# Optimization experiments

Measured on AMD Instinct MI355X. Metric: run time of the kernel, lower is better.

Reference implementation:

```python
import jax, jax.numpy as jnp
import numpy as np

BIG = 1e10  # sentinel depth for empty pixels


def setup_inputs() -> dict:
    key = jax.random.key(0)
    k1, k2, k3, k4, k5 = jax.random.split(key, 5)
    N, C = 200000, 64
    B, H, W = 4, 376, 1241
    features = jax.random.normal(k1, (N, C), dtype=jnp.float32)
    # coordinates: [batch_id, z, y, x]; grid is ~67 bins per axis given
    # voxel_size=0.75 and pcd_range [0,-25,-25,50,25,25]
    b = jax.random.randint(k2, (N, 1), 0, B, dtype=jnp.int32)
    z = jax.random.randint(k3, (N, 1), 0, 67, dtype=jnp.int32)
    y = jax.random.randint(k4, (N, 1), 0, 67, dtype=jnp.int32)
    x = jax.random.randint(k5, (N, 1), 0, 67, dtype=jnp.int32)
    coordinates = jnp.concatenate([b, z, y, x], axis=1)
    # KITTI-like pinhole intrinsics
    K = jnp.array([[721.5377, 0.0, 609.5593],
                   [0.0, 721.5377, 172.854],
                   [0.0, 0.0, 1.0]], dtype=jnp.float32)
    return {"features": features, "coordinates": coordinates, "K": K,
            "batch_size": B, "h": H, "w": W}


def _projection_matrix(K):
    # module-constant R and V2P (from __init__ defaults)
    R = jnp.array([[0., -1., 0.], [0., 0., -1.], [1., 0., 0.]], dtype=jnp.float32)
    vx = vy = vz = 0.75
    x_off = vx / 2 + 0.0
    y_off = vy / 2 + (-25.0)
    z_off = vz / 2 + (-25.0)
    V2P = jnp.array([[vx, 0., 0., x_off],
                     [0., vy, 0., y_off],
                     [0., 0., vz, z_off]], dtype=jnp.float32)
    return K @ R @ V2P  # [3,4]


def reference(features, coordinates, K, batch_size, h, w):
    N, C = features.shape
    P = _projection_matrix(K)  # [3,4]
    b = coordinates[:, 0]
    # coordinates order is [batch_id, z, y, x]; homogeneous point is [x,y,z,1]
    xyz1 = jnp.stack([coordinates[:, 3], coordinates[:, 2], coordinates[:, 1],
                      jnp.ones_like(coordinates[:, 0])], axis=1).astype(jnp.float32)
    p = xyz1 @ P.T  # [N,3]
    depth = p[:, 2]
    safe_d = jnp.where(depth > 1e-6, depth, 1.0)
    u = jnp.floor(p[:, 0] / safe_d).astype(jnp.int32)
    v = jnp.floor(p[:, 1] / safe_d).astype(jnp.int32)
    valid = (depth > 1e-6) & (u >= 0) & (u < w) & (v >= 0) & (v < h)
    num_pix = batch_size * h * w
    pix = jnp.where(valid, b * (h * w) + v * w + u, 0)
    d = jnp.where(valid, depth, BIG)
    # z-buffer: min depth per pixel, then winning voxel index (tie -> smallest idx)
    min_depth = jnp.full((num_pix,), BIG, dtype=jnp.float32).at[pix].min(d)
    is_win = valid & (d <= min_depth[pix])
    cand = jnp.where(is_win, jnp.arange(N, dtype=jnp.int32), N)
    win_idx = jnp.full((num_pix,), N, dtype=jnp.int32).at[pix].min(cand)
    feats_pad = jnp.concatenate([features, jnp.zeros((1, C), features.dtype)], axis=0)
    out = feats_pad[win_idx].reshape(batch_size, h, w, C).transpose(0, 3, 1, 2)  # [B,C,H,W]
    inv_depth = jnp.where(min_depth < BIG, 1.0 / min_depth, 0.0).reshape(batch_size, h, w)
    return out, inv_depth
```

## Files before the change

### kernel.cpp

```cpp
#include <hip/hip_runtime.h>
#include <cstdint>
#include <cstddef>

constexpr int Bc = 4;
constexpr int Hc = 376;
constexpr int Wc = 1241;
constexpr int Cc = 64;
constexpr int HW = Hc * Wc;
constexpr int NUM_PIX = Bc * HW;


__global__ void init_entries(uint4* __restrict__ p, int n16) {
    int t = blockIdx.x * blockDim.x + threadIdx.x;
    if (t < n16) p[t] = make_uint4(0xFFFFFFFFu, 0xFFFFFFFFu, 0xFFFFFFFFu, 0xFFFFFFFFu);
}

__global__ void scatter_points(const int* __restrict__ coords,
                               const float* __restrict__ Km,
                               unsigned long long* __restrict__ entries,
                               int N) {
    int n = blockIdx.x * blockDim.x + threadIdx.x;
    if (n >= N) return;

    const int4 co = *(const int4*)(coords + 4 * (size_t)n);
    const int   bi = co.x;
    const float zf = (float)co.y;
    const float yf = (float)co.z;
    const float xf = (float)co.w;

    float P0[4], P1[4], P2[4];
    {
        const float xo = 0.375f, yo = -24.625f, zo = -24.625f;
        float KR0, KR1, KR2;
        KR0 = Km[2]; KR1 = -Km[0]; KR2 = -Km[1];
        P0[0] = __fmaf_rn(KR0, 0.75f, 0.0f);
        P0[1] = __fmaf_rn(KR1, 0.75f, 0.0f);
        P0[2] = __fmaf_rn(KR2, 0.75f, 0.0f);
        P0[3] = __fmaf_rn(KR2, zo, __fmaf_rn(KR1, yo, __fmaf_rn(KR0, xo, 0.0f)));
        KR0 = Km[5]; KR1 = -Km[3]; KR2 = -Km[4];
        P1[0] = __fmaf_rn(KR0, 0.75f, 0.0f);
        P1[1] = __fmaf_rn(KR1, 0.75f, 0.0f);
        P1[2] = __fmaf_rn(KR2, 0.75f, 0.0f);
        P1[3] = __fmaf_rn(KR2, zo, __fmaf_rn(KR1, yo, __fmaf_rn(KR0, xo, 0.0f)));
        KR0 = Km[8]; KR1 = -Km[6]; KR2 = -Km[7];
        P2[0] = __fmaf_rn(KR0, 0.75f, 0.0f);
        P2[1] = __fmaf_rn(KR1, 0.75f, 0.0f);
        P2[2] = __fmaf_rn(KR2, 0.75f, 0.0f);
        P2[3] = __fmaf_rn(KR2, zo, __fmaf_rn(KR1, yo, __fmaf_rn(KR0, xo, 0.0f)));
    }

    float p0 = __fmaf_rn(1.0f, P0[3], __fmaf_rn(zf, P0[2], __fmaf_rn(yf, P0[1], __fmaf_rn(xf, P0[0], 0.0f))));
    float p1 = __fmaf_rn(1.0f, P1[3], __fmaf_rn(zf, P1[2], __fmaf_rn(yf, P1[1], __fmaf_rn(xf, P1[0], 0.0f))));
    float depth = __fmaf_rn(1.0f, P2[3], __fmaf_rn(zf, P2[2], __fmaf_rn(yf, P2[1], __fmaf_rn(xf, P2[0], 0.0f))));

    const bool dok = depth > 1e-6f;
    const float safe_d = dok ? depth : 1.0f;
    const int u = (int)floorf(__fdiv_rn(p0, safe_d));
    const int v = (int)floorf(__fdiv_rn(p1, safe_d));

    if (dok && u >= 0 && u < Wc && v >= 0 && v < Hc && bi >= 0 && bi < Bc) {
        const int pix = bi * HW + v * Wc + u;
        const unsigned long long key =
            ((unsigned long long)__float_as_uint(depth) << 32) | (unsigned int)n;
        atomicMin(&entries[pix], key);
    }
}

__global__ void decode_entries(const unsigned long long* __restrict__ entries,
                               int* __restrict__ widx,
                               float* __restrict__ inv_depth) {
    int t = blockIdx.x * blockDim.x + threadIdx.x;
    if (t >= NUM_PIX) return;
    const unsigned long long e = entries[t];
    int idx = -1;
    float inv = 0.0f;
    if (e != ~0ULL) {
        idx = (int)(unsigned int)(e & 0xFFFFFFFFu);
        const float dep = __uint_as_float((unsigned int)(e >> 32));
        inv = __fdiv_rn(1.0f, dep);
    }
    widx[t] = idx;
    inv_depth[t] = inv;
}

__global__ void gather_features(const int* __restrict__ widx,
                                const float* __restrict__ feat,
                                float* __restrict__ out) {
    const int q = blockIdx.x * blockDim.x + threadIdx.x;
    if (q >= HW / 4) return;
    const int c = blockIdx.y;
    const int b = blockIdx.z;
    const int local = q * 4;

    const int4 i4 = *(const int4*)(widx + (size_t)b * HW + local);
    float4 o;
    o.x = (i4.x < 0) ? 0.0f : feat[(size_t)i4.x * Cc + c];
    o.y = (i4.y < 0) ? 0.0f : feat[(size_t)i4.y * Cc + c];
    o.z = (i4.z < 0) ? 0.0f : feat[(size_t)i4.z * Cc + c];
    o.w = (i4.w < 0) ? 0.0f : feat[(size_t)i4.w * Cc + c];

    *(float4*)(out + ((size_t)(b * Cc + c) * HW + local)) = o;
}

extern "C" void kernel_launch(void* const* d_in, const int* in_sizes, int n_in,
                              void* d_out, int out_size, void* d_ws, size_t ws_size,
                              hipStream_t stream) {
    const float* features = (const float*)d_in[0];
    const int*   coords   = (const int*)d_in[1];
    const float* Km       = (const float*)d_in[2];
    const int N = in_sizes[1] / 4;

    unsigned long long* entries = (unsigned long long*)d_ws;
    int* widx = (int*)((char*)d_ws + (size_t)NUM_PIX * 8);

    float* out_feat = (float*)d_out;
    float* out_inv  = (float*)d_out + (size_t)Bc * Cc * HW;

    const int n16 = NUM_PIX / 2;
    init_entries<<<(n16 + 255) / 256, 256, 0, stream>>>((uint4*)entries, n16);

    scatter_points<<<(N + 255) / 256, 256, 0, stream>>>(coords, Km, entries, N);

    decode_entries<<<(NUM_PIX + 255) / 256, 256, 0, stream>>>(entries, widx, out_inv);

    dim3 ggrid((HW / 4 + 255) / 256, Cc, Bc);
    gather_features<<<ggrid, 256, 0, stream>>>(widx, features, out_feat);
}
```

Measured before the change: 528.9 us.

## Fuse decode and gather, loading full feature rows per pixel

Merges the decode kernel into the gather kernel so the winning index is read straight from the packed depth/index entries, with no intermediate index buffer. Each thread now handles four pixels across all 64 channels, loading feature rows as float4 and transposing them into channel-major float4 stores, where before the grid was split per channel with scalar gathers. This cuts index re-reads and launch count, and replaces 64 strided scalar loads per pixel with contiguous row loads. In exchange each thread does more work, uses more registers, and the grid has far fewer blocks.

```diff
diff --git a/kernel.cpp b/kernel.cpp
--- a/kernel.cpp
+++ b/kernel.cpp
@@ -66,40 +66,47 @@
     }
 }
 
-__global__ void decode_entries(const unsigned long long* __restrict__ entries,
-                               int* __restrict__ widx,
-                               float* __restrict__ inv_depth) {
-    int t = blockIdx.x * blockDim.x + threadIdx.x;
-    if (t >= NUM_PIX) return;
-    const unsigned long long e = entries[t];
-    int idx = -1;
-    float inv = 0.0f;
-    if (e != ~0ULL) {
-        idx = (int)(unsigned int)(e & 0xFFFFFFFFu);
-        const float dep = __uint_as_float((unsigned int)(e >> 32));
-        inv = __fdiv_rn(1.0f, dep);
-    }
-    widx[t] = idx;
-    inv_depth[t] = inv;
-}
-
-__global__ void gather_features(const int* __restrict__ widx,
-                                const float* __restrict__ feat,
-                                float* __restrict__ out) {
+__global__ void decode_gather(const unsigned long long* __restrict__ entries,
+                              const float* __restrict__ feat,
+                              float* __restrict__ out_feat,
+                              float* __restrict__ out_inv) {
     const int q = blockIdx.x * blockDim.x + threadIdx.x;
     if (q >= HW / 4) return;
-    const int c = blockIdx.y;
-    const int b = blockIdx.z;
+    const int b = blockIdx.y;
     const int local = q * 4;
+    const size_t pixbase = (size_t)b * HW + local;
 
-    const int4 i4 = *(const int4*)(widx + (size_t)b * HW + local);
-    float4 o;
-    o.x = (i4.x < 0) ? 0.0f : feat[(size_t)i4.x * Cc + c];
-    o.y = (i4.y < 0) ? 0.0f : feat[(size_t)i4.y * Cc + c];
-    o.z = (i4.z < 0) ? 0.0f : feat[(size_t)i4.z * Cc + c];
-    o.w = (i4.w < 0) ? 0.0f : feat[(size_t)i4.w * Cc + c];
+    const unsigned long long e0 = entries[pixbase + 0];
+    const unsigned long long e1 = entries[pixbase + 1];
+    const unsigned long long e2 = entries[pixbase + 2];
+    const unsigned long long e3 = entries[pixbase + 3];
 
-    *(float4*)(out + ((size_t)(b * Cc + c) * HW + local)) = o;
+    int   i0 = -1, i1 = -1, i2 = -1, i3 = -1;
+    float v0 = 0.0f, v1 = 0.0f, v2 = 0.0f, v3 = 0.0f;
+    if (e0 != ~0ULL) { i0 = (int)(unsigned int)(e0 & 0xFFFFFFFFu); v0 = __fdiv_rn(1.0f, __uint_as_float((unsigned int)(e0 >> 32))); }
+    if (e1 != ~0ULL) { i1 = (int)(unsigned int)(e1 & 0xFFFFFFFFu); v1 = __fdiv_rn(1.0f, __uint_as_float((unsigned int)(e1 >> 32))); }
+    if (e2 != ~0ULL) { i2 = (int)(unsigned int)(e2 & 0xFFFFFFFFu); v2 = __fdiv_rn(1.0f, __uint_as_float((unsigned int)(e2 >> 32))); }
+    if (e3 != ~0ULL) { i3 = (int)(unsigned int)(e3 & 0xFFFFFFFFu); v3 = __fdiv_rn(1.0f, __uint_as_float((unsigned int)(e3 >> 32))); }
+
+    *(float4*)(out_inv + pixbase) = make_float4(v0, v1, v2, v3);
+
+    float* ob = out_feat + ((size_t)b * Cc) * HW + local;
+    const float4 z4 = make_float4(0.0f, 0.0f, 0.0f, 0.0f);
+
+#pragma unroll
+    for (int cg = 0; cg < 16; ++cg) {
+        const int c0 = cg * 4;
+        const float4 r0 = (i0 < 0) ? z4 : *(const float4*)(feat + (size_t)i0 * Cc + c0);
+        const float4 r1 = (i1 < 0) ? z4 : *(const float4*)(feat + (size_t)i1 * Cc + c0);
+        const float4 r2 = (i2 < 0) ? z4 : *(const float4*)(feat + (size_t)i2 * Cc + c0);
+        const float4 r3 = (i3 < 0) ? z4 : *(const float4*)(feat + (size_t)i3 * Cc + c0);
+
+        float* p = ob + (size_t)c0 * HW;
+        *(float4*)(p)                = make_float4(r0.x, r1.x, r2.x, r3.x);
+        *(float4*)(p + HW)           = make_float4(r0.y, r1.y, r2.y, r3.y);
+        *(float4*)(p + 2 * (size_t)HW) = make_float4(r0.z, r1.z, r2.z, r3.z);
+        *(float4*)(p + 3 * (size_t)HW) = make_float4(r0.w, r1.w, r2.w, r3.w);
+    }
 }
 
 extern "C" void kernel_launch(void* const* d_in, const int* in_sizes, int n_in,
@@ -111,7 +118,6 @@
     const int N = in_sizes[1] / 4;
 
     unsigned long long* entries = (unsigned long long*)d_ws;
-    int* widx = (int*)((char*)d_ws + (size_t)NUM_PIX * 8);
 
     float* out_feat = (float*)d_out;
     float* out_inv  = (float*)d_out + (size_t)Bc * Cc * HW;
@@ -121,8 +127,6 @@
 
     scatter_points<<<(N + 255) / 256, 256, 0, stream>>>(coords, Km, entries, N);
 
-    decode_entries<<<(NUM_PIX + 255) / 256, 256, 0, stream>>>(entries, widx, out_inv);
-
-    dim3 ggrid((HW / 4 + 255) / 256, Cc, Bc);
-    gather_features<<<ggrid, 256, 0, stream>>>(widx, features, out_feat);
+    dim3 ggrid((HW / 4 + 255) / 256, Bc);
+    decode_gather<<<ggrid, 256, 0, stream>>>(entries, features, out_feat, out_inv);
 }
```

Result: slower. 568.7 us (+7.5%).
